# Performance work log

Hardware: AMD Instinct MI355X
Metric: run time of the kernel (lower is better)

## Reference

```python
import jax, jax.numpy as jnp
import numpy as np

D_DISP = 20   # module arg d
S1 = 1        # module arg s1
WIN = D_DISP + S1


def setup_inputs() -> dict:
    key = jax.random.key(0)
    k1, k2 = jax.random.split(key)
    x1 = jax.random.normal(k1, (4, 128, 128, 128), dtype=jnp.float32)
    x2 = jax.random.normal(k2, (4, 128, 128, 128), dtype=jnp.float32)
    return {"x1": x1, "x2": x2}


def reference(x1, x2):
    b, c, w, h = x1.shape
    pad = D_DISP // 2
    # original code calls .detach() on the unfolded x2 patches
    x2p = jax.lax.stop_gradient(
        jnp.pad(x2, ((0, 0), (0, 0), (pad, pad), (pad, pad)))
    )  # [b, c, w+2*pad, h+2*pad]

    uv = jnp.arange(WIN * WIN)

    def step(carry, uv_i):
        u = uv_i // WIN
        v = uv_i % WIN
        win = jax.lax.dynamic_slice(x2p, (0, 0, u, v), (b, c, w, h))
        return carry, jnp.sum(x1 * win, axis=1)  # [b, w, h]

    _, out = jax.lax.scan(step, None, uv)
    return jnp.transpose(out, (1, 0, 2, 3))
```

## Files before the change

### kernel.cpp

```cpp
#include <hip/hip_runtime.h>

#define BATCH 4
#define CH    128
#define HW    128
#define PAD   10
#define PW    148
#define PWC   160
#define WIN   21
#define NUV   441

typedef short s16x8 __attribute__((ext_vector_type(8)));
typedef float f32x4 __attribute__((ext_vector_type(4)));
typedef unsigned short u16x4 __attribute__((ext_vector_type(4)));

static __device__ __forceinline__ unsigned short f32_to_bf16(float f) {
    unsigned int u = __float_as_uint(f);
    u += 0x7FFFu + ((u >> 16) & 1u);
    return (unsigned short)(u >> 16);
}

__global__ __launch_bounds__(256) void corr_transpose_kernel(
    const float* __restrict__ x1, const float* __restrict__ x2,
    unsigned short* __restrict__ x1b, unsigned short* __restrict__ x2b)
{
    __shared__ float lds[32][34];
    int bidx = blockIdx.x;
    int which = (bidx >= 8192) ? 1 : 0;
    if (which) bidx -= 8192;
    int tjt = bidx & 3;
    int tct = (bidx >> 2) & 3;
    int i   = (bidx >> 4) & 127;
    int b   = bidx >> 11;
    int c0 = tct * 32, j0 = tjt * 32;
    int t  = threadIdx.x;

    const float* __restrict__ src = which ? x2 : x1;

    int cl = t >> 3, jq = t & 7;
    float4 vv = *(const float4*)&src[(((size_t)b * CH + c0 + cl) * HW + i) * HW + j0 + jq * 4];
    lds[cl][jq * 4 + 0] = vv.x;
    lds[cl][jq * 4 + 1] = vv.y;
    lds[cl][jq * 4 + 2] = vv.z;
    lds[cl][jq * 4 + 3] = vv.w;
    __syncthreads();

    int jl = t >> 3, cg = t & 7;
    u16x4 o;
    o[0] = f32_to_bf16(lds[cg * 4 + 0][jl]);
    o[1] = f32_to_bf16(lds[cg * 4 + 1][jl]);
    o[2] = f32_to_bf16(lds[cg * 4 + 2][jl]);
    o[3] = f32_to_bf16(lds[cg * 4 + 3][jl]);
    int j = j0 + jl, c = c0 + cg * 4;
    if (!which) {
        *(u16x4*)&x1b[(((size_t)b * HW + i) * HW + j) * CH + c] = o;
    } else {
        *(u16x4*)&x2b[(((size_t)b * PW + i + PAD) * PWC + (j + PAD)) * CH + c] = o;
    }
}

__global__ __launch_bounds__(256, 2) void corr_mfma_kernel(
    const unsigned short* __restrict__ x1b,
    const unsigned short* __restrict__ x2b,
    float* __restrict__ out)
{
    __shared__ unsigned short ldsA[64 * 128];
    __shared__ unsigned short ldsB[4 * 48 * 128];

    int bid  = blockIdx.x;
    int swz  = (bid & 7) * 768 + (bid >> 3);
    int z    = swz % 6;
    int rest = swz / 6;
    int tj   = rest & 7;
    int ti   = (rest >> 3) & 31;
    int b    = rest >> 8;
    int i0 = ti * 4, j0 = tj * 16;

    int t    = threadIdx.x;
    int lane = t & 63;
    int w    = t >> 6;
    int l15  = lane & 15;
    int lhi  = lane >> 4;
    int rr   = z * 4 + w;

    #pragma unroll
    for (int it = 0; it < 4; ++it) {
        int s   = w * 4 + it;
        int dpi = s >> 2;
        int pl  = lane >> 4;
        int hs  = lane & 15;
        int p   = s * 4 + pl;
        int dpj = (s & 3) * 4 + pl;
        int h   = hs ^ (p & 7);
        const unsigned short* srcp =
            x1b + (((size_t)b * HW + i0 + dpi) * HW + j0 + dpj) * CH + h * 8;
        __builtin_amdgcn_global_load_lds(
            (const __attribute__((address_space(1))) void*)srcp,
            (__attribute__((address_space(3))) void*)(ldsA + s * 512),
            16, 0, 0);
    }

    const unsigned short* rowbase =
        x2b + (((size_t)b * PW + i0 + rr) * PWC + j0) * CH;
    unsigned short* myB = ldsB + w * (48 * 128);
    #pragma unroll
    for (int g = 0; g < 12; ++g) {
        int ql = lane >> 4;
        int hs = lane & 15;
        int q  = g * 4 + ql;
        int h  = hs ^ (q & 7);
        const unsigned short* srcp = rowbase + (size_t)q * CH + h * 8;
        __builtin_amdgcn_global_load_lds(
            (const __attribute__((address_space(1))) void*)srcp,
            (__attribute__((address_space(3))) void*)(myB + g * 512),
            16, 0, 0);
    }

    __syncthreads();

    f32x4 acc[3][4];
    #pragma unroll
    for (int ntl = 0; ntl < 3; ++ntl)
        #pragma unroll
        for (int mt = 0; mt < 4; ++mt)
            acc[ntl][mt] = (f32x4)(0.0f);

    #pragma unroll
    for (int kc = 0; kc < 4; ++kc) {
        int slotoff = ((kc * 4 + lhi) ^ (l15 & 7)) * 8;
        s16x8 a[4], bb[3];
        #pragma unroll
        for (int mt = 0; mt < 4; ++mt)
            a[mt] = *(const s16x8*)(ldsA + (mt * 16 + l15) * 128 + slotoff);
        #pragma unroll
        for (int ntl = 0; ntl < 3; ++ntl)
            bb[ntl] = *(const s16x8*)(myB + (ntl * 16 + l15) * 128 + slotoff);
        #pragma unroll
        for (int ntl = 0; ntl < 3; ++ntl)
            #pragma unroll
            for (int mt = 0; mt < 4; ++mt)
                acc[ntl][mt] = __builtin_amdgcn_mfma_f32_16x16x32_bf16(a[mt], bb[ntl], acc[ntl][mt], 0, 0, 0);
    }

    float (*myCT)[20] = (float(*)[20])myB;
    #pragma unroll
    for (int dpi = 0; dpi < 4; ++dpi) {
        int u = rr - dpi;
        if ((unsigned)u < 21u) {
            int r2 = i0 + dpi + u - PAD;
            #pragma unroll
            for (int ntl = 0; ntl < 3; ++ntl)
                *(f32x4*)&myCT[ntl * 16 + l15][lhi * 4] = acc[ntl][dpi];
            #pragma unroll
            for (int vb = 0; vb < 6; ++vb) {
                int v = vb * 4 + lhi;
                if (v < 21) {
                    int c2 = j0 + l15 + v - PAD;
                    float val = myCT[l15 + v][l15];
                    if ((unsigned)r2 >= 128u || (unsigned)c2 >= 128u) val = 0.0f;
                    out[(((size_t)b * NUV + u * WIN + v) * HW + (i0 + dpi)) * HW + j0 + l15] = val;
                }
            }
        }
    }
}

extern "C" void kernel_launch(void* const* d_in, const int* in_sizes, int n_in,
                              void* d_out, int out_size, void* d_ws, size_t ws_size,
                              hipStream_t stream) {
    const float* x1 = (const float*)d_in[0];
    const float* x2 = (const float*)d_in[1];
    float* out = (float*)d_out;

    const size_t X1B_ELEMS = (size_t)BATCH * HW * HW * CH;
    const size_t X2B_ELEMS = (size_t)BATCH * PW * PWC * CH;
    if (ws_size < (X1B_ELEMS + X2B_ELEMS) * sizeof(unsigned short)) return;

    unsigned short* x1b = (unsigned short*)d_ws;
    unsigned short* x2b = x1b + X1B_ELEMS;

    corr_transpose_kernel<<<16384, 256, 0, stream>>>(x1, x2, x1b, x2b);
    corr_mfma_kernel<<<6144, 256, 0, stream>>>(x1b, x2b, out);
}
```

Measured before the change: 61.72 us.

## Shrink per-wave B tile to 36 rows, raise occupancy, widen transpose stores

The MFMA kernel now loads only 36 padded x2 columns per wave instead of 48. The third N-tile overlaps the second (row offsets 0, 16, 20), which cuts LDS use and global loads so three blocks fit per CU. MFMA issue is bracketed with s_setprio to favour the matrix instructions. The transpose kernel handles all 128 channels per block with 16-byte bf16 stores and a quarter of the blocks, reducing launch and store overhead. The overlapping tile computes some columns twice and needs per-row swizzle index math.

```diff
diff --git a/kernel.cpp b/kernel.cpp
--- a/kernel.cpp
+++ b/kernel.cpp
@@ -8,10 +8,11 @@
 #define PWC   160
 #define WIN   21
 #define NUV   441
+#define NQ    36
 
 typedef short s16x8 __attribute__((ext_vector_type(8)));
 typedef float f32x4 __attribute__((ext_vector_type(4)));
-typedef unsigned short u16x4 __attribute__((ext_vector_type(4)));
+typedef unsigned short u16x8 __attribute__((ext_vector_type(8)));
 
 static __device__ __forceinline__ unsigned short f32_to_bf16(float f) {
     unsigned int u = __float_as_uint(f);
@@ -23,48 +24,51 @@
     const float* __restrict__ x1, const float* __restrict__ x2,
     unsigned short* __restrict__ x1b, unsigned short* __restrict__ x2b)
 {
-    __shared__ float lds[32][34];
-    int bidx = blockIdx.x;
-    int which = (bidx >= 8192) ? 1 : 0;
-    if (which) bidx -= 8192;
-    int tjt = bidx & 3;
-    int tct = (bidx >> 2) & 3;
-    int i   = (bidx >> 4) & 127;
-    int b   = bidx >> 11;
-    int c0 = tct * 32, j0 = tjt * 32;
+    __shared__ float lds[128][33];
+    int bidx  = blockIdx.x;
+    int which = bidx >= 2048;
+    if (which) bidx -= 2048;
+    int jt = bidx & 3;
+    int i  = (bidx >> 2) & 127;
+    int b  = bidx >> 9;
+    int j0 = jt * 32;
     int t  = threadIdx.x;
 
     const float* __restrict__ src = which ? x2 : x1;
 
     int cl = t >> 3, jq = t & 7;
-    float4 vv = *(const float4*)&src[(((size_t)b * CH + c0 + cl) * HW + i) * HW + j0 + jq * 4];
-    lds[cl][jq * 4 + 0] = vv.x;
-    lds[cl][jq * 4 + 1] = vv.y;
-    lds[cl][jq * 4 + 2] = vv.z;
-    lds[cl][jq * 4 + 3] = vv.w;
+    #pragma unroll
+    for (int it = 0; it < 4; ++it) {
+        int c = it * 32 + cl;
+        float4 vv = *(const float4*)&src[(((size_t)b * CH + c) * HW + i) * HW + j0 + jq * 4];
+        lds[c][jq * 4 + 0] = vv.x;
+        lds[c][jq * 4 + 1] = vv.y;
+        lds[c][jq * 4 + 2] = vv.z;
+        lds[c][jq * 4 + 3] = vv.w;
+    }
     __syncthreads();
 
-    int jl = t >> 3, cg = t & 7;
-    u16x4 o;
-    o[0] = f32_to_bf16(lds[cg * 4 + 0][jl]);
-    o[1] = f32_to_bf16(lds[cg * 4 + 1][jl]);
-    o[2] = f32_to_bf16(lds[cg * 4 + 2][jl]);
-    o[3] = f32_to_bf16(lds[cg * 4 + 3][jl]);
-    int j = j0 + jl, c = c0 + cg * 4;
-    if (!which) {
-        *(u16x4*)&x1b[(((size_t)b * HW + i) * HW + j) * CH + c] = o;
-    } else {
-        *(u16x4*)&x2b[(((size_t)b * PW + i + PAD) * PWC + (j + PAD)) * CH + c] = o;
+    int jl = t >> 4, cg = t & 15;
+    #pragma unroll
+    for (int it = 0; it < 2; ++it) {
+        int j = it * 16 + jl;
+        u16x8 o;
+        #pragma unroll
+        for (int k = 0; k < 8; ++k) o[k] = f32_to_bf16(lds[cg * 8 + k][j]);
+        if (!which)
+            *(u16x8*)&x1b[(((size_t)b * HW + i) * HW + j0 + j) * CH + cg * 8] = o;
+        else
+            *(u16x8*)&x2b[(((size_t)b * PW + i + PAD) * PWC + (j0 + j + PAD)) * CH + cg * 8] = o;
     }
 }
 
-__global__ __launch_bounds__(256, 2) void corr_mfma_kernel(
+__global__ __launch_bounds__(256, 3) void corr_mfma_kernel(
     const unsigned short* __restrict__ x1b,
     const unsigned short* __restrict__ x2b,
     float* __restrict__ out)
 {
     __shared__ unsigned short ldsA[64 * 128];
-    __shared__ unsigned short ldsB[4 * 48 * 128];
+    __shared__ unsigned short ldsB[4 * NQ * 128];
 
     int bid  = blockIdx.x;
     int swz  = (bid & 7) * 768 + (bid >> 3);
@@ -101,9 +105,9 @@
 
     const unsigned short* rowbase =
         x2b + (((size_t)b * PW + i0 + rr) * PWC + j0) * CH;
-    unsigned short* myB = ldsB + w * (48 * 128);
+    unsigned short* myB = ldsB + w * (NQ * 128);
     #pragma unroll
-    for (int g = 0; g < 12; ++g) {
+    for (int g = 0; g < 9; ++g) {
         int ql = lane >> 4;
         int hs = lane & 15;
         int q  = g * 4 + ql;
@@ -124,21 +128,29 @@
         for (int mt = 0; mt < 4; ++mt)
             acc[ntl][mt] = (f32x4)(0.0f);
 
+    const int q0tab[3] = {0, 16, 20};
+
     #pragma unroll
     for (int kc = 0; kc < 4; ++kc) {
-        int slotoff = ((kc * 4 + lhi) ^ (l15 & 7)) * 8;
         s16x8 a[4], bb[3];
         #pragma unroll
-        for (int mt = 0; mt < 4; ++mt)
-            a[mt] = *(const s16x8*)(ldsA + (mt * 16 + l15) * 128 + slotoff);
+        for (int mt = 0; mt < 4; ++mt) {
+            int slot = (kc * 4 + lhi) ^ (l15 & 7);
+            a[mt] = *(const s16x8*)(ldsA + (mt * 16 + l15) * 128 + slot * 8);
+        }
         #pragma unroll
-        for (int ntl = 0; ntl < 3; ++ntl)
-            bb[ntl] = *(const s16x8*)(myB + (ntl * 16 + l15) * 128 + slotoff);
+        for (int ntl = 0; ntl < 3; ++ntl) {
+            int q    = q0tab[ntl] + l15;
+            int slot = (kc * 4 + lhi) ^ (q & 7);
+            bb[ntl] = *(const s16x8*)(myB + q * 128 + slot * 8);
+        }
+        __builtin_amdgcn_s_setprio(1);
         #pragma unroll
         for (int ntl = 0; ntl < 3; ++ntl)
             #pragma unroll
             for (int mt = 0; mt < 4; ++mt)
                 acc[ntl][mt] = __builtin_amdgcn_mfma_f32_16x16x32_bf16(a[mt], bb[ntl], acc[ntl][mt], 0, 0, 0);
+        __builtin_amdgcn_s_setprio(0);
     }
 
     float (*myCT)[20] = (float(*)[20])myB;
@@ -149,7 +161,7 @@
             int r2 = i0 + dpi + u - PAD;
             #pragma unroll
             for (int ntl = 0; ntl < 3; ++ntl)
-                *(f32x4*)&myCT[ntl * 16 + l15][lhi * 4] = acc[ntl][dpi];
+                *(f32x4*)&myCT[q0tab[ntl] + l15][lhi * 4] = acc[ntl][dpi];
             #pragma unroll
             for (int vb = 0; vb < 6; ++vb) {
                 int v = vb * 4 + lhi;
@@ -178,6 +190,6 @@
     unsigned short* x1b = (unsigned short*)d_ws;
     unsigned short* x2b = x1b + X1B_ELEMS;
 
-    corr_transpose_kernel<<<16384, 256, 0, stream>>>(x1, x2, x1b, x2b);
+    corr_transpose_kernel<<<4096, 256, 0, stream>>>(x1, x2, x1b, x2b);
     corr_mfma_kernel<<<6144, 256, 0, stream>>>(x1b, x2b, out);
 }
```

After: 54.45 us. -11.8%, faster.
